# Optimization experiments

Measured on AMD Instinct MI355X. Metric: run time of the kernel, lower is better.

The kernel has to match this reference:

```python
import jax, jax.numpy as jnp
import numpy as np

D_MODEL = 2048
N_HEADS = 32
N_KV_HEADS = 8
HEAD_DIM = D_MODEL // N_HEADS
ROPE_BASE = 10000.0

def setup_inputs() -> dict:
    key = jax.random.key(0)
    ks = jax.random.split(key, 5)
    B, S = 1, 2048
    x = jax.random.normal(ks[0], (B, S, D_MODEL), dtype=jnp.float32)
    sc = 1.0 / np.sqrt(D_MODEL)
    Wq = jax.random.normal(ks[1], (D_MODEL, D_MODEL), dtype=jnp.float32) * sc
    Wk = jax.random.normal(ks[2], (N_KV_HEADS * HEAD_DIM, D_MODEL), dtype=jnp.float32) * sc
    Wv = jax.random.normal(ks[3], (N_KV_HEADS * HEAD_DIM, D_MODEL), dtype=jnp.float32) * sc
    Wo = jax.random.normal(ks[4], (D_MODEL, D_MODEL), dtype=jnp.float32) * sc
    return {"x": x, "Wq": Wq, "Wk": Wk, "Wv": Wv, "Wo": Wo}

def _rope_cos_sin(seq_len, dtype):
    inv_freq = 1.0 / (ROPE_BASE ** (jnp.arange(0, HEAD_DIM, 2, dtype=jnp.float32) / HEAD_DIM))
    t = jnp.arange(seq_len, dtype=jnp.float32)
    freqs = jnp.einsum('i,j->ij', t, inv_freq)          # [S, hd/2]
    emb = jnp.concatenate([freqs, freqs], axis=-1)      # [S, hd]
    return jnp.cos(emb).astype(dtype), jnp.sin(emb).astype(dtype)

def _rotate_half(x):
    x1, x2 = x[..., : HEAD_DIM // 2], x[..., HEAD_DIM // 2 :]
    return jnp.concatenate([-x2, x1], axis=-1)

def reference(x, Wq, Wk, Wv, Wo):
    B, S, _ = x.shape
    scale = HEAD_DIM ** -0.5
    # projections (Linear: x @ W.T)
    q = (x @ Wq.T).reshape(B, S, N_HEADS, HEAD_DIM).transpose(0, 2, 1, 3)      # [B,H,S,hd]
    k = (x @ Wk.T).reshape(B, S, N_KV_HEADS, HEAD_DIM).transpose(0, 2, 1, 3)   # [B,Hkv,S,hd]
    v = (x @ Wv.T).reshape(B, S, N_KV_HEADS, HEAD_DIM).transpose(0, 2, 1, 3)
    cos, sin = _rope_cos_sin(S, x.dtype)                # [S,hd], broadcasts over B,H
    q = q * cos + _rotate_half(q) * sin
    k = k * cos + _rotate_half(k) * sin
    rep = N_HEADS // N_KV_HEADS
    k = jnp.repeat(k, rep, axis=1)                       # [B,H,S,hd]
    v = jnp.repeat(v, rep, axis=1)
    scores = jnp.einsum('bhqd,bhkd->bhqk', q, k) * scale # [B,H,S,S]
    attn = jax.nn.softmax(scores, axis=-1)
    out = jnp.einsum('bhqk,bhkd->bhqd', attn, v)         # [B,H,S,hd]
    out = out.transpose(0, 2, 1, 3).reshape(B, S, D_MODEL)
    return out @ Wo.T
```

## Files before the change

kernel.cpp:

```cpp
#include <hip/hip_runtime.h>
#include <hip/hip_bf16.h>
#include <cmath>

typedef __bf16 bf16_t;
typedef __attribute__((ext_vector_type(8))) __bf16 bf16x8;
typedef __attribute__((ext_vector_type(4))) float f32x4;
typedef __attribute__((ext_vector_type(4))) short s16x4;

#define S_LEN 2048
#define DMODEL 2048
#define KVDIM 512
#define NHEADS 32
#define NKV 8
#define HDIM 64

__device__ inline f32x4 zero4() { f32x4 z; z[0]=0.f; z[1]=0.f; z[2]=0.f; z[3]=0.f; return z; }

__global__ void convert_all(const float* __restrict__ s0, bf16_t* __restrict__ d0,
                            const float* __restrict__ s1, bf16_t* __restrict__ d1,
                            const float* __restrict__ s2, bf16_t* __restrict__ d2,
                            const float* __restrict__ s3, bf16_t* __restrict__ d3,
                            const float* __restrict__ s4, bf16_t* __restrict__ d4) {
  int b = blockIdx.x;
  const float* src; bf16_t* dst; int boff;
  if      (b < 2048) { src = s0; dst = d0; boff = b; }
  else if (b < 4096) { src = s1; dst = d1; boff = b - 2048; }
  else if (b < 4608) { src = s2; dst = d2; boff = b - 4096; }
  else if (b < 5120) { src = s3; dst = d3; boff = b - 4608; }
  else               { src = s4; dst = d4; boff = b - 5120; }
  int idx = (boff * 256 + threadIdx.x) * 8;
  bf16x8 v;
#pragma unroll
  for (int j = 0; j < 8; j++) v[j] = (bf16_t)src[idx + j];
  *(bf16x8*)(dst + idx) = v;
}

template <int BN, bool F32OUT>
__device__ __forceinline__ void gemm_core(const bf16_t* __restrict__ A,
                                          const bf16_t* __restrict__ Bt,
                                          void* __restrict__ Cout,
                                          int N, int K, int bm, int bn) {
  constexpr int NT_W = BN / 32;
  __shared__ __attribute__((aligned(16))) bf16_t As[128 * 64];
  __shared__ __attribute__((aligned(16))) bf16_t Bs[BN * 64];
  const int tid  = threadIdx.x;
  const int wave = tid >> 6, lane = tid & 63;
  const int wm = wave >> 1, wn = wave & 1;
  const int quad = lane >> 4, lr = lane & 15;
  const int srow = lane >> 3, scol = lane & 7;

  f32x4 acc[4][NT_W];
#pragma unroll
  for (int i = 0; i < 4; i++)
#pragma unroll
    for (int j = 0; j < NT_W; j++) acc[i][j] = zero4();

  for (int k0 = 0; k0 < K; k0 += 64) {
#pragma unroll
    for (int i = 0; i < 4; i++) {
      const bf16_t* gA = A + (size_t)(bm + i * 32 + wave * 8 + srow) * K + k0 + scol * 8;
      bf16_t* lA = As + (i * 32 + wave * 8) * 64;
      __builtin_amdgcn_global_load_lds((const __attribute__((address_space(1))) void*)gA,
                                       (__attribute__((address_space(3))) void*)lA, 16, 0, 0);
    }
#pragma unroll
    for (int i = 0; i < BN / 32; i++) {
      const bf16_t* gB = Bt + (size_t)(bn + i * 32 + wave * 8 + srow) * K + k0 + scol * 8;
      bf16_t* lB = Bs + (i * 32 + wave * 8) * 64;
      __builtin_amdgcn_global_load_lds((const __attribute__((address_space(1))) void*)gB,
                                       (__attribute__((address_space(3))) void*)lB, 16, 0, 0);
    }
    __syncthreads();
#pragma unroll
    for (int ks = 0; ks < 2; ks++) {
      bf16x8 a[4], b[NT_W];
#pragma unroll
      for (int mt = 0; mt < 4; mt++)
        a[mt] = *(const bf16x8*)&As[(wm * 64 + mt * 16 + lr) * 64 + ks * 32 + quad * 8];
#pragma unroll
      for (int nt = 0; nt < NT_W; nt++)
        b[nt] = *(const bf16x8*)&Bs[(wn * (BN / 2) + nt * 16 + lr) * 64 + ks * 32 + quad * 8];
#pragma unroll
      for (int mt = 0; mt < 4; mt++)
#pragma unroll
        for (int nt = 0; nt < NT_W; nt++)
          acc[mt][nt] = __builtin_amdgcn_mfma_f32_16x16x32_bf16(a[mt], b[nt], acc[mt][nt], 0, 0, 0);
    }
    __syncthreads();
  }

#pragma unroll
  for (int mt = 0; mt < 4; mt++)
#pragma unroll
    for (int nt = 0; nt < NT_W; nt++)
#pragma unroll
      for (int r = 0; r < 4; r++) {
        int row = bm + wm * 64 + mt * 16 + quad * 4 + r;
        int col = bn + wn * (BN / 2) + nt * 16 + lr;
        if (F32OUT) ((float*)Cout)[(size_t)row * N + col] = acc[mt][nt][r];
        else ((bf16_t*)Cout)[(size_t)row * N + col] = (bf16_t)acc[mt][nt][r];
      }
}

__global__ __launch_bounds__(256) void gemm_proj(const bf16_t* __restrict__ xb,
                                                 const bf16_t* __restrict__ Wqb,
                                                 const bf16_t* __restrict__ Wkb,
                                                 const bf16_t* __restrict__ Wvb,
                                                 bf16_t* __restrict__ qb,
                                                 bf16_t* __restrict__ kb,
                                                 bf16_t* __restrict__ vb) {
  int b = blockIdx.x;
  if (b < 512) {
    gemm_core<64, false>(xb, Wqb, qb, 2048, 2048, (b >> 5) * 128, (b & 31) * 64);
  } else if (b < 640) {
    int r = b - 512;
    gemm_core<64, false>(xb, Wkb, kb, 512, 2048, (r >> 3) * 128, (r & 7) * 64);
  } else {
    int r = b - 640;
    gemm_core<64, false>(Wvb, xb, vb, 2048, 2048, (r >> 5) * 128, (r & 31) * 64);
  }
}

__global__ __launch_bounds__(256) void gemm_out(const bf16_t* __restrict__ A,
                                                const bf16_t* __restrict__ Bt,
                                                float* __restrict__ C) {
  int b = blockIdx.x;
  gemm_core<64, true>(A, Bt, C, 2048, 2048, (b >> 5) * 128, (b & 31) * 64);
}

__global__ void rope_k(bf16_t* __restrict__ kb) {
  int idx = blockIdx.x * 256 + threadIdx.x;
  int s = idx >> 8;
  int rem = idx & 255;
  int head = rem >> 5;
  int i = rem & 31;
  float freq = __expf(-0.2878231366f * (float)i);
  float ang = (float)s * freq;
  float sn, cs;
  sincosf(ang, &sn, &cs);
  size_t base = (size_t)s * KVDIM + head * 64 + i;
  float x0 = (float)kb[base];
  float x1 = (float)kb[base + 32];
  kb[base]      = (bf16_t)(x0 * cs - x1 * sn);
  kb[base + 32] = (bf16_t)(x1 * cs + x0 * sn);
}

__global__ __launch_bounds__(256) void attn_kernel(const bf16_t* __restrict__ q,
                                                   const bf16_t* __restrict__ k,
                                                   const bf16_t* __restrict__ vT,
                                                   bf16_t* __restrict__ out) {
  __shared__ __attribute__((aligned(16))) bf16_t Ks[128 * 64];
  __shared__ __attribute__((aligned(16))) bf16_t Vs[64 * 128];
  const int tid  = threadIdx.x;
  const int wave = tid >> 6, lane = tid & 63;
  const int quad = lane >> 4, lr = lane & 15;
  const int srow = lane >> 3, scol = lane & 7;
  const int vrow = lane >> 4, vcol = lane & 15;
  const int cg = scol ^ srow;
  const int qt = blockIdx.x, h = blockIdx.y;
  const int hkv = h >> 2;
  const int qrow0 = qt * 64 + wave * 16;
  const int sw = lr & 7;
  const int c0 = (quad ^ sw) * 8;
  const int c1 = ((quad + 4) ^ sw) * 8;

  bf16x8 aq0, aq1;
  {
    const bf16_t* qp = q + (size_t)(qrow0 + lr) * DMODEL + h * HDIM + quad * 8;
    bf16x8 r0 = *(const bf16x8*)qp;
    bf16x8 r1 = *(const bf16x8*)(qp + 32);
    float srow_f = (float)(qrow0 + lr);
#pragma unroll
    for (int j = 0; j < 8; j++) {
      float freq = __expf(-0.2878231366f * (float)(quad * 8 + j));
      float sn, cs;
      sincosf(srow_f * freq, &sn, &cs);
      float x0 = (float)r0[j], x1 = (float)r1[j];
      aq0[j] = (bf16_t)(x0 * cs - x1 * sn);
      aq1[j] = (bf16_t)(x1 * cs + x0 * sn);
    }
  }

  f32x4 O[4];
  float l_lane = 0.f;
#pragma unroll
  for (int mt = 0; mt < 4; mt++) O[mt] = zero4();

  for (int kt = 0; kt < S_LEN; kt += 128) {
#pragma unroll
    for (int j = 0; j < 4; j++) {
      const bf16_t* gK = k + (size_t)(kt + wave * 32 + j * 8 + srow) * KVDIM + hkv * HDIM + cg * 8;
      bf16_t* lK = Ks + (wave * 32 + j * 8) * 64;
      __builtin_amdgcn_global_load_lds((const __attribute__((address_space(1))) void*)gK,
                                       (__attribute__((address_space(3))) void*)lK, 16, 0, 0);
    }
#pragma unroll
    for (int j = 0; j < 4; j++) {
      int dg = wave * 16 + j * 4 + vrow;
      int cgv = vcol ^ (dg & 7);
      const bf16_t* gV = vT + (size_t)(hkv * HDIM + dg) * S_LEN + kt + cgv * 8;
      bf16_t* lV = Vs + (wave * 16 + j * 4) * 128;
      __builtin_amdgcn_global_load_lds((const __attribute__((address_space(1))) void*)gV,
                                       (__attribute__((address_space(3))) void*)lV, 16, 0, 0);
    }
    __syncthreads();

    f32x4 sc[8];
#pragma unroll
    for (int nt = 0; nt < 8; nt++) sc[nt] = zero4();
#pragma unroll
    for (int nt = 0; nt < 8; nt++) {
      const int rk = (nt * 16 + lr) * 64;
      bf16x8 kb0 = *(const bf16x8*)&Ks[rk + c0];
      bf16x8 kb1 = *(const bf16x8*)&Ks[rk + c1];
      sc[nt] = __builtin_amdgcn_mfma_f32_16x16x32_bf16(kb0, aq0, sc[nt], 0, 0, 0);
      sc[nt] = __builtin_amdgcn_mfma_f32_16x16x32_bf16(kb1, aq1, sc[nt], 0, 0, 0);
    }
    s16x4 bp[8];
#pragma unroll
    for (int nt = 0; nt < 8; nt++) {
#pragma unroll
      for (int r = 0; r < 4; r++) {
        float p = __expf(sc[nt][r] * 0.125f);
        l_lane += p;
        bf16_t pb = (bf16_t)p;
        bp[nt][r] = __builtin_bit_cast(short, pb);
      }
    }
#pragma unroll
    for (int nt = 0; nt < 8; nt++) {
      const int slot = ((nt * 2 + (quad >> 1)) ^ sw) * 8 + (quad & 1) * 4;
      s16x4 av[4];
#pragma unroll
      for (int mt = 0; mt < 4; mt++)
        av[mt] = *(const s16x4*)&Vs[(mt * 16 + lr) * 128 + slot];
#pragma unroll
      for (int mt = 0; mt < 4; mt++)
        O[mt] = __builtin_amdgcn_mfma_f32_16x16x16bf16_1k(av[mt], bp[nt], O[mt], 0, 0, 0);
    }
    __syncthreads();
  }

  l_lane += __shfl_xor(l_lane, 16);
  l_lane += __shfl_xor(l_lane, 32);
  float inv_l = 1.f / l_lane;

#pragma unroll
  for (int mt = 0; mt < 4; mt++) {
    s16x4 ov;
#pragma unroll
    for (int r = 0; r < 4; r++) {
      bf16_t b = (bf16_t)(O[mt][r] * inv_l);
      ov[r] = __builtin_bit_cast(short, b);
    }
    *(s16x4*)&out[(size_t)(qrow0 + lr) * DMODEL + h * HDIM + mt * 16 + quad * 4] = ov;
  }
}

extern "C" void kernel_launch(void* const* d_in, const int* in_sizes, int n_in,
                              void* d_out, int out_size, void* d_ws, size_t ws_size,
                              hipStream_t stream) {
  (void)in_sizes; (void)n_in; (void)out_size; (void)ws_size;
  const float* x  = (const float*)d_in[0];
  const float* Wq = (const float*)d_in[1];
  const float* Wk = (const float*)d_in[2];
  const float* Wv = (const float*)d_in[3];
  const float* Wo = (const float*)d_in[4];

  bf16_t* xb  = (bf16_t*)d_ws;
  bf16_t* Wqb = xb  + (size_t)4 * 1024 * 1024;
  bf16_t* Wkb = Wqb + (size_t)4 * 1024 * 1024;
  bf16_t* Wvb = Wkb + (size_t)1024 * 1024;
  bf16_t* qb  = Wvb + (size_t)1024 * 1024;
  bf16_t* kb  = qb  + (size_t)4 * 1024 * 1024;
  bf16_t* vb  = kb  + (size_t)1024 * 1024;
  bf16_t* Wob = vb  + (size_t)1024 * 1024;
  bf16_t* ab  = xb;

  dim3 blk(256);
  convert_all<<<7168, blk, 0, stream>>>(x, xb, Wq, Wqb, Wk, Wkb, Wv, Wvb, Wo, Wob);
  gemm_proj<<<768, blk, 0, stream>>>(xb, Wqb, Wkb, Wvb, qb, kb, vb);
  rope_k<<<2048, blk, 0, stream>>>(kb);
  attn_kernel<<<dim3(S_LEN / 64, NHEADS), blk, 0, stream>>>(qb, kb, vb, ab);
  gemm_out<<<512, blk, 0, stream>>>(ab, Wob, (float*)d_out);
}
```

Before: 241.1 us.

## Split attention over the key dimension in two halves and add a combine kernel

The attention kernel now splits the key/value sequence into two halves along a new grid dimension. Each half writes an unnormalized partial output and its row sums, and a new combine kernel adds the partials and normalizes them. The key tile also shrinks from 128 to 64 rows with a simpler V load layout, and V fragments are preloaded before the PV MFMAs. This doubles the block count (1024 to 2048) to fill more CUs and cuts shared memory per block, at the cost of an extra kernel launch, partial buffers passing through global memory, and bf16 rounding of the partial sums.

```diff
diff --git a/kernel.cpp b/kernel.cpp
--- a/kernel.cpp
+++ b/kernel.cpp
@@ -148,16 +148,17 @@
 __global__ __launch_bounds__(256) void attn_kernel(const bf16_t* __restrict__ q,
                                                    const bf16_t* __restrict__ k,
                                                    const bf16_t* __restrict__ vT,
-                                                   bf16_t* __restrict__ out) {
-  __shared__ __attribute__((aligned(16))) bf16_t Ks[128 * 64];
-  __shared__ __attribute__((aligned(16))) bf16_t Vs[64 * 128];
+                                                   bf16_t* __restrict__ Op0,
+                                                   bf16_t* __restrict__ Op1,
+                                                   float* __restrict__ lpart) {
+  __shared__ __attribute__((aligned(16))) bf16_t Ks[64 * 64];
+  __shared__ __attribute__((aligned(16))) bf16_t Vs[64 * 64];
   const int tid  = threadIdx.x;
   const int wave = tid >> 6, lane = tid & 63;
   const int quad = lane >> 4, lr = lane & 15;
   const int srow = lane >> 3, scol = lane & 7;
-  const int vrow = lane >> 4, vcol = lane & 15;
   const int cg = scol ^ srow;
-  const int qt = blockIdx.x, h = blockIdx.y;
+  const int qt = blockIdx.x, h = blockIdx.y, z = blockIdx.z;
   const int hkv = h >> 2;
   const int qrow0 = qt * 64 + wave * 16;
   const int sw = lr & 7;
@@ -186,39 +187,43 @@
 #pragma unroll
   for (int mt = 0; mt < 4; mt++) O[mt] = zero4();
 
-  for (int kt = 0; kt < S_LEN; kt += 128) {
-#pragma unroll
-    for (int j = 0; j < 4; j++) {
-      const bf16_t* gK = k + (size_t)(kt + wave * 32 + j * 8 + srow) * KVDIM + hkv * HDIM + cg * 8;
-      bf16_t* lK = Ks + (wave * 32 + j * 8) * 64;
+  const int kt0 = z * (S_LEN / 2);
+  for (int kt = kt0; kt < kt0 + S_LEN / 2; kt += 64) {
+#pragma unroll
+    for (int j = 0; j < 2; j++) {
+      const bf16_t* gK = k + (size_t)(kt + wave * 16 + j * 8 + srow) * KVDIM + hkv * HDIM + cg * 8;
+      bf16_t* lK = Ks + (wave * 16 + j * 8) * 64;
       __builtin_amdgcn_global_load_lds((const __attribute__((address_space(1))) void*)gK,
                                        (__attribute__((address_space(3))) void*)lK, 16, 0, 0);
-    }
-#pragma unroll
-    for (int j = 0; j < 4; j++) {
-      int dg = wave * 16 + j * 4 + vrow;
-      int cgv = vcol ^ (dg & 7);
-      const bf16_t* gV = vT + (size_t)(hkv * HDIM + dg) * S_LEN + kt + cgv * 8;
-      bf16_t* lV = Vs + (wave * 16 + j * 4) * 128;
+      const bf16_t* gV = vT + (size_t)(hkv * HDIM + wave * 16 + j * 8 + srow) * S_LEN + kt + cg * 8;
+      bf16_t* lV = Vs + (wave * 16 + j * 8) * 64;
       __builtin_amdgcn_global_load_lds((const __attribute__((address_space(1))) void*)gV,
                                        (__attribute__((address_space(3))) void*)lV, 16, 0, 0);
     }
     __syncthreads();
 
-    f32x4 sc[8];
-#pragma unroll
-    for (int nt = 0; nt < 8; nt++) sc[nt] = zero4();
-#pragma unroll
-    for (int nt = 0; nt < 8; nt++) {
+    f32x4 sc[4];
+#pragma unroll
+    for (int nt = 0; nt < 4; nt++) sc[nt] = zero4();
+#pragma unroll
+    for (int nt = 0; nt < 4; nt++) {
       const int rk = (nt * 16 + lr) * 64;
       bf16x8 kb0 = *(const bf16x8*)&Ks[rk + c0];
       bf16x8 kb1 = *(const bf16x8*)&Ks[rk + c1];
       sc[nt] = __builtin_amdgcn_mfma_f32_16x16x32_bf16(kb0, aq0, sc[nt], 0, 0, 0);
       sc[nt] = __builtin_amdgcn_mfma_f32_16x16x32_bf16(kb1, aq1, sc[nt], 0, 0, 0);
     }
-    s16x4 bp[8];
-#pragma unroll
-    for (int nt = 0; nt < 8; nt++) {
+    s16x4 av[4][4];
+#pragma unroll
+    for (int nt = 0; nt < 4; nt++) {
+      const int slot = ((nt * 2 + (quad >> 1)) ^ sw) * 8 + (quad & 1) * 4;
+#pragma unroll
+      for (int mt = 0; mt < 4; mt++)
+        av[nt][mt] = *(const s16x4*)&Vs[(mt * 16 + lr) * 64 + slot];
+    }
+    s16x4 bp[4];
+#pragma unroll
+    for (int nt = 0; nt < 4; nt++) {
 #pragma unroll
       for (int r = 0; r < 4; r++) {
         float p = __expf(sc[nt][r] * 0.125f);
@@ -228,33 +233,48 @@
       }
     }
 #pragma unroll
-    for (int nt = 0; nt < 8; nt++) {
-      const int slot = ((nt * 2 + (quad >> 1)) ^ sw) * 8 + (quad & 1) * 4;
-      s16x4 av[4];
+    for (int nt = 0; nt < 4; nt++)
 #pragma unroll
       for (int mt = 0; mt < 4; mt++)
-        av[mt] = *(const s16x4*)&Vs[(mt * 16 + lr) * 128 + slot];
-#pragma unroll
-      for (int mt = 0; mt < 4; mt++)
-        O[mt] = __builtin_amdgcn_mfma_f32_16x16x16bf16_1k(av[mt], bp[nt], O[mt], 0, 0, 0);
-    }
+        O[mt] = __builtin_amdgcn_mfma_f32_16x16x16bf16_1k(av[nt][mt], bp[nt], O[mt], 0, 0, 0);
     __syncthreads();
   }
 
   l_lane += __shfl_xor(l_lane, 16);
   l_lane += __shfl_xor(l_lane, 32);
-  float inv_l = 1.f / l_lane;
+  bf16_t* Op = z ? Op1 : Op0;
+  if (quad == 0) lpart[(size_t)z * 65536 + h * 2048 + qrow0 + lr] = l_lane;
 
 #pragma unroll
   for (int mt = 0; mt < 4; mt++) {
     s16x4 ov;
 #pragma unroll
     for (int r = 0; r < 4; r++) {
-      bf16_t b = (bf16_t)(O[mt][r] * inv_l);
+      bf16_t b = (bf16_t)O[mt][r];
       ov[r] = __builtin_bit_cast(short, b);
     }
-    *(s16x4*)&out[(size_t)(qrow0 + lr) * DMODEL + h * HDIM + mt * 16 + quad * 4] = ov;
-  }
+    *(s16x4*)&Op[(size_t)(qrow0 + lr) * DMODEL + h * HDIM + mt * 16 + quad * 4] = ov;
+  }
+}
+
+__global__ void combine_kernel(const bf16_t* __restrict__ Op0,
+                               const bf16_t* __restrict__ Op1,
+                               const float* __restrict__ lpart,
+                               bf16_t* __restrict__ ab) {
+  int idx = blockIdx.x * 256 + threadIdx.x;
+  int row = idx >> 8;
+  int col = (idx & 255) * 8;
+  int h = col >> 6;
+  float l0 = lpart[h * 2048 + row];
+  float l1 = lpart[65536 + h * 2048 + row];
+  float inv = 1.f / (l0 + l1);
+  size_t off = (size_t)row * DMODEL + col;
+  bf16x8 a = *(const bf16x8*)(Op0 + off);
+  bf16x8 b = *(const bf16x8*)(Op1 + off);
+  bf16x8 o;
+#pragma unroll
+  for (int j = 0; j < 8; j++) o[j] = (bf16_t)(((float)a[j] + (float)b[j]) * inv);
+  *(bf16x8*)(ab + off) = o;
 }
 
 extern "C" void kernel_launch(void* const* d_in, const int* in_sizes, int n_in,
@@ -275,12 +295,16 @@
   bf16_t* kb  = qb  + (size_t)4 * 1024 * 1024;
   bf16_t* vb  = kb  + (size_t)1024 * 1024;
   bf16_t* Wob = vb  + (size_t)1024 * 1024;
-  bf16_t* ab  = xb;
+  bf16_t* Op0 = xb;
+  bf16_t* Op1 = Wqb;
+  float*  lpart = (float*)Wkb;
+  bf16_t* ab  = qb;
 
   dim3 blk(256);
   convert_all<<<7168, blk, 0, stream>>>(x, xb, Wq, Wqb, Wk, Wkb, Wv, Wvb, Wo, Wob);
   gemm_proj<<<768, blk, 0, stream>>>(xb, Wqb, Wkb, Wvb, qb, kb, vb);
   rope_k<<<2048, blk, 0, stream>>>(kb);
-  attn_kernel<<<dim3(S_LEN / 64, NHEADS), blk, 0, stream>>>(qb, kb, vb, ab);
+  attn_kernel<<<dim3(S_LEN / 64, NHEADS, 2), blk, 0, stream>>>(qb, kb, vb, Op0, Op1, lpart);
+  combine_kernel<<<2048, blk, 0, stream>>>(Op0, Op1, lpart, ab);
   gemm_out<<<512, blk, 0, stream>>>(ab, Wob, (float*)d_out);
 }
```

New measurement: 246.6 us. 2.3% more time.
